# Kernel tuning notes

Hardware: AMD Instinct MI355X
Metric: run time of the kernel (lower is better)

The kernel has to match this reference:

```python
import jax, jax.numpy as jnp
import numpy as np

# 8 fixed 3x3 shift-and-subtract kernels (center -1, one neighbor +1)
_KERNELS = np.array([
    [[1, 0, 0], [0, -1, 0], [0, 0, 0]],
    [[0, 1, 0], [0, -1, 0], [0, 0, 0]],
    [[0, 0, 1], [0, -1, 0], [0, 0, 0]],
    [[0, 0, 0], [1, -1, 0], [0, 0, 0]],
    [[0, 0, 0], [0, -1, 1], [0, 0, 0]],
    [[0, 0, 0], [0, -1, 0], [1, 0, 0]],
    [[0, 0, 0], [0, -1, 0], [0, 1, 0]],
    [[0, 0, 0], [0, -1, 0], [0, 0, 1]],
], dtype=np.float32)  # [8,3,3]


def contrast_depth_conv(x):
    # x: [B, H, W] single-channel depth map.
    # torch does groups=8 depthwise conv on the input broadcast to 8 channels,
    # which is identical to a 1->8 channel VALID conv with the 8 kernels.
    w = jnp.asarray(_KERNELS)[:, None, :, :]  # [8,1,3,3] OIHW
    y = jax.lax.conv_general_dilated(
        x[:, None, :, :],  # [B,1,H,W] NCHW
        w,
        window_strides=(1, 1),
        padding='VALID',
        dimension_numbers=('NCHW', 'OIHW', 'NCHW'),
    )
    return y  # [B, 8, H-2, W-2]


def setup_inputs() -> dict:
    key = jax.random.key(0)
    k1, k2 = jax.random.split(key)
    B, H, W = 16384, 32, 32
    out = jax.random.normal(k1, (B, H, W), dtype=jnp.float32)
    label = jax.random.normal(k2, (B, H, W), dtype=jnp.float32)
    return {"out": out, "label": label}


def reference(out, label):
    c_out = contrast_depth_conv(out)      # [B,8,30,30]
    c_label = contrast_depth_conv(label)  # [B,8,30,30]
    diff = c_out - c_label
    return jnp.mean(diff * diff)
```

## Files before the change

kernel.cpp:

```cpp
#include <hip/hip_runtime.h>


#define THREADS 256
#define IPB 8
#define STRIDE 36

__global__ __launch_bounds__(THREADS, 8) void cdl_partial(
    const float* __restrict__ outp,
    const float* __restrict__ labp,
    float* __restrict__ partial,
    int nimg)
{
    __shared__ float d[2][32][STRIDE];
    const int t   = threadIdx.x;
    const int row = t >> 3;
    const int col = (t & 7) << 2;

    const int b0 = blockIdx.x * IPB;
    const float4* op = (const float4*)outp + (long long)b0 * 256 + t;
    const float4* lp = (const float4*)labp + (long long)b0 * 256 + t;

    const bool active = t < 225;
    const int qy = t / 15, qx = t - qy * 15;
    const int ry = 2 * qy, cx = 2 * qx;

    float acc = 0.f;

    float4 o = *op, l = *lp;
    float4 dv = make_float4(o.x - l.x, o.y - l.y, o.z - l.z, o.w - l.w);

    const int n = (nimg - b0 < IPB) ? (nimg - b0) : IPB;
    for (int i = 0; i < n; ++i) {
        float4 on, ln;
        const bool more = (i + 1 < n);
        if (more) { on = op[(i + 1) * 256]; ln = lp[(i + 1) * 256]; }

        *(float4*)&d[i & 1][row][col] = dv;
        __syncthreads();

        if (active) {
            const float (*im)[STRIDE] = d[i & 1];
            float dd[4][4];
            #pragma unroll
            for (int r = 0; r < 4; ++r) {
                const float2 a = *(const float2*)&im[ry + r][cx];
                const float2 b = *(const float2*)&im[ry + r][cx + 2];
                dd[r][0] = a.x; dd[r][1] = a.y; dd[r][2] = b.x; dd[r][3] = b.y;
            }
            #pragma unroll
            for (int cyy = 0; cyy < 2; ++cyy) {
                #pragma unroll
                for (int cxx = 0; cxx < 2; ++cxx) {
                    const float c = dd[cyy + 1][cxx + 1];
                    #pragma unroll
                    for (int ny = 0; ny < 3; ++ny) {
                        #pragma unroll
                        for (int nx = 0; nx < 3; ++nx) {
                            if (ny == 1 && nx == 1) continue;
                            const float v = dd[cyy + ny][cxx + nx] - c;
                            acc += v * v;
                        }
                    }
                }
            }
        }

        if (more)
            dv = make_float4(on.x - ln.x, on.y - ln.y, on.z - ln.z, on.w - ln.w);
    }

    #pragma unroll
    for (int off = 32; off; off >>= 1) acc += __shfl_down(acc, off, 64);
    __shared__ float red[4];
    const int lane = t & 63, wid = t >> 6;
    if (lane == 0) red[wid] = acc;
    __syncthreads();
    if (t == 0) partial[blockIdx.x] = red[0] + red[1] + red[2] + red[3];
}

__global__ __launch_bounds__(THREADS) void cdl_final(
    const float* __restrict__ partial,
    float* __restrict__ out,
    int np,
    float inv_count)
{
    __shared__ float red[THREADS / 64];
    const int t = threadIdx.x;
    float acc = 0.f;
    for (int i = t; i < np; i += THREADS) acc += partial[i];
    #pragma unroll
    for (int off = 32; off; off >>= 1) acc += __shfl_down(acc, off, 64);
    if ((t & 63) == 0) red[t >> 6] = acc;
    __syncthreads();
    if (t == 0) out[0] = (red[0] + red[1] + red[2] + red[3]) * inv_count;
}

extern "C" void kernel_launch(void* const* d_in, const int* in_sizes, int n_in,
                              void* d_out, int out_size, void* d_ws, size_t ws_size,
                              hipStream_t stream) {
    const float* outp = (const float*)d_in[0];
    const float* labp = (const float*)d_in[1];
    float* partial = (float*)d_ws;
    const int nimg = in_sizes[0] / 1024;
    const int nblocks = (nimg + IPB - 1) / IPB;
    const float inv_count = 1.0f / ((float)nimg * 8.0f * 900.0f);

    cdl_partial<<<nblocks, THREADS, 0, stream>>>(outp, labp, partial, nimg);
    cdl_final<<<1, THREADS, 0, stream>>>(partial, (float*)d_out, nblocks, inv_count);
}
```

Baseline: 29.39 us.

## Drop LDS staging; load overlapping 4x4 patches directly from global memory

Removes the shared-memory double buffer and per-image __syncthreads; each of the 225 active threads now reads its 4x4 patch of both inputs straight from global memory with float2 loads, relying on cache for the overlap between neighbouring patches. Launch bounds drop from 8 to 2 waves per EU, allowing more registers, and the image loop is unrolled by 2 for memory-level parallelism. This trades barrier and LDS traffic for redundant, less coalesced global/L1 accesses (each element is read up to four times) and possibly lower occupancy.

```diff
diff --git a/kernel.cpp b/kernel.cpp
--- a/kernel.cpp
+++ b/kernel.cpp
@@ -3,70 +3,61 @@
 
 #define THREADS 256
 #define IPB 8
-#define STRIDE 36
 
-__global__ __launch_bounds__(THREADS, 8) void cdl_partial(
+__global__ __launch_bounds__(THREADS, 2) void cdl_partial(
     const float* __restrict__ outp,
     const float* __restrict__ labp,
     float* __restrict__ partial,
     int nimg)
 {
-    __shared__ float d[2][32][STRIDE];
-    const int t   = threadIdx.x;
-    const int row = t >> 3;
-    const int col = (t & 7) << 2;
-
-    const int b0 = blockIdx.x * IPB;
-    const float4* op = (const float4*)outp + (long long)b0 * 256 + t;
-    const float4* lp = (const float4*)labp + (long long)b0 * 256 + t;
-
-    const bool active = t < 225;
-    const int qy = t / 15, qx = t - qy * 15;
-    const int ry = 2 * qy, cx = 2 * qx;
-
+    const int t = threadIdx.x;
     float acc = 0.f;
 
-    float4 o = *op, l = *lp;
-    float4 dv = make_float4(o.x - l.x, o.y - l.y, o.z - l.z, o.w - l.w);
+    if (t < 225) {
+        const int qy = t / 15, qx = t - qy * 15;
+        const long long base = (long long)blockIdx.x * IPB * 1024
+                             + (2 * qy) * 32 + 2 * qx;
+        const float* ob = outp + base;
+        const float* lb = labp + base;
+        const int n = (nimg - blockIdx.x * IPB < IPB) ? (nimg - blockIdx.x * IPB) : IPB;
 
-    const int n = (nimg - b0 < IPB) ? (nimg - b0) : IPB;
-    for (int i = 0; i < n; ++i) {
-        float4 on, ln;
-        const bool more = (i + 1 < n);
-        if (more) { on = op[(i + 1) * 256]; ln = lp[(i + 1) * 256]; }
-
-        *(float4*)&d[i & 1][row][col] = dv;
-        __syncthreads();
-
-        if (active) {
-            const float (*im)[STRIDE] = d[i & 1];
+        #pragma unroll 2
+        for (int i = 0; i < n; ++i) {
+            const float* o = ob + i * 1024;
+            const float* l = lb + i * 1024;
+            float2 ov[4][2], lv[4][2];
+            #pragma unroll
+            for (int r = 0; r < 4; ++r) {
+                ov[r][0] = *(const float2*)(o + r * 32);
+                ov[r][1] = *(const float2*)(o + r * 32 + 2);
+                lv[r][0] = *(const float2*)(l + r * 32);
+                lv[r][1] = *(const float2*)(l + r * 32 + 2);
+            }
             float dd[4][4];
             #pragma unroll
             for (int r = 0; r < 4; ++r) {
-                const float2 a = *(const float2*)&im[ry + r][cx];
-                const float2 b = *(const float2*)&im[ry + r][cx + 2];
-                dd[r][0] = a.x; dd[r][1] = a.y; dd[r][2] = b.x; dd[r][3] = b.y;
+                dd[r][0] = ov[r][0].x - lv[r][0].x;
+                dd[r][1] = ov[r][0].y - lv[r][0].y;
+                dd[r][2] = ov[r][1].x - lv[r][1].x;
+                dd[r][3] = ov[r][1].y - lv[r][1].y;
             }
             #pragma unroll
-            for (int cyy = 0; cyy < 2; ++cyy) {
+            for (int cy = 1; cy <= 2; ++cy) {
                 #pragma unroll
-                for (int cxx = 0; cxx < 2; ++cxx) {
-                    const float c = dd[cyy + 1][cxx + 1];
+                for (int cx = 1; cx <= 2; ++cx) {
+                    const float c = dd[cy][cx];
                     #pragma unroll
-                    for (int ny = 0; ny < 3; ++ny) {
+                    for (int ny = -1; ny <= 1; ++ny) {
                         #pragma unroll
-                        for (int nx = 0; nx < 3; ++nx) {
-                            if (ny == 1 && nx == 1) continue;
-                            const float v = dd[cyy + ny][cxx + nx] - c;
+                        for (int nx = -1; nx <= 1; ++nx) {
+                            if (ny == 0 && nx == 0) continue;
+                            const float v = dd[cy + ny][cx + nx] - c;
                             acc += v * v;
                         }
                     }
                 }
             }
         }
-
-        if (more)
-            dv = make_float4(on.x - ln.x, on.y - ln.y, on.z - ln.z, on.w - ln.w);
     }
 
     #pragma unroll
```

Measured after the change: 28.54 us. -2.9%, faster.
